# Kernel optimization log

Hardware: AMD Instinct MI355X
Metric: run time of the kernel (lower is better)

## Reference

```python
import jax, jax.numpy as jnp
import numpy as np

N, NFEAT, HID, NHEADS, NCLASS = 6144, 128, 128, 8, 40
SMOOTH = 0.5   # smoo init arg of GC_withres
ALPHA = 0.2    # LeakyReLU negative slope (pyGAT default)
EPS = 1e-5     # BatchNorm eps
NEG = -9e15    # masked-attention fill value


def setup_inputs() -> dict:
    key = jax.random.key(0)
    ks = jax.random.split(key, 20)
    x = jax.random.normal(ks[0], (N, NFEAT), dtype=jnp.float32)
    # sparse-ish symmetric normalized adjacency (~12 avg degree + self loops)
    m = (jax.random.uniform(ks[1], (N, N)) < 0.001).astype(jnp.float32)
    a = jnp.maximum(m, m.T) + jnp.eye(N, dtype=jnp.float32)
    dinv = 1.0 / jnp.sqrt(jnp.sum(a, axis=1))
    adj = a * dinv[:, None] * dinv[None, :]
    W_att = jax.random.normal(ks[2], (NHEADS, NFEAT, HID), dtype=jnp.float32) * 0.1
    a_src = jax.random.normal(ks[3], (NHEADS, HID), dtype=jnp.float32) * 0.1
    a_dst = jax.random.normal(ks[4], (NHEADS, HID), dtype=jnp.float32) * 0.1
    bn0_g = jnp.ones((NFEAT,), jnp.float32)
    bn0_b = jnp.zeros((NFEAT,), jnp.float32)
    bn0_m = jax.random.normal(ks[5], (NFEAT,), dtype=jnp.float32) * 0.1
    bn0_v = 1.0 + 0.1 * jax.random.uniform(ks[6], (NFEAT,), dtype=jnp.float32)
    bn1_g = jnp.ones((HID,), jnp.float32)
    bn1_b = jnp.zeros((HID,), jnp.float32)
    bn1_m = jax.random.normal(ks[7], (HID,), dtype=jnp.float32) * 0.1
    bn1_v = 1.0 + 0.1 * jax.random.uniform(ks[8], (HID,), dtype=jnp.float32)
    gc_w = jax.random.normal(ks[9], (HID * NHEADS, NCLASS), dtype=jnp.float32) * 0.05
    gc_b = jnp.zeros((NCLASS,), jnp.float32)
    return {"x": x, "adj": adj, "W_att": W_att, "a_src": a_src, "a_dst": a_dst,
            "bn0_g": bn0_g, "bn0_b": bn0_b, "bn0_m": bn0_m, "bn0_v": bn0_v,
            "bn1_g": bn1_g, "bn1_b": bn1_b, "bn1_m": bn1_m, "bn1_v": bn1_v,
            "gc_w": gc_w, "gc_b": gc_b}


def _bn(x, g, b, m, v):
    # BatchNorm1d in eval mode: normalize with running stats
    return (x - m) * (g / jnp.sqrt(v + EPS)) + b


def reference(x, adj, W_att, a_src, a_dst, bn0_g, bn0_b, bn0_m, bn0_v,
              bn1_g, bn1_b, bn1_m, bn1_v, gc_w, gc_b):
    x = _bn(x, bn0_g, bn0_b, bn0_m, bn0_v)          # bn0; dropout identity (eval)
    mask = adj > 0
    head_outs = []
    for h in range(NHEADS):                          # fixed small head count
        Wh = x @ W_att[h]                            # [N, HID]
        s1 = Wh @ a_src[h]                           # [N]
        s2 = Wh @ a_dst[h]                           # [N]
        e = jax.nn.leaky_relu(s1[:, None] + s2[None, :], ALPHA)  # [N, N]
        att = jax.nn.softmax(jnp.where(mask, e, NEG), axis=1)    # softmax over nbrs
        h_prime = att @ Wh                           # aggregate
        head_outs.append(jax.nn.relu(_bn(h_prime, bn1_g, bn1_b, bn1_m, bn1_v)))
    xcat = jnp.concatenate(head_outs, axis=1)        # [N, HID*NHEADS]
    # GC_withres: (smooth * A @ (XW) + XW) / (1 + smooth) + bias
    support = xcat @ gc_w                            # [N, NCLASS]
    out = (SMOOTH * (adj @ support) + support) / (1.0 + SMOOTH) + gc_b
    return jax.nn.log_softmax(out, axis=1)
```

## Files before the change

kernel.cpp:

```cpp
#include <hip/hip_runtime.h>
#include <math.h>

#define N      6144
#define NFEAT  128
#define HID    128
#define NHEADS 8
#define NCLASS 40
#define CAP    96
#define EPS    1e-5f
#define ALPHA  0.2f

typedef short bf16x8 __attribute__((ext_vector_type(8)));
typedef float f32x4  __attribute__((ext_vector_type(4)));

__device__ inline float bf2f(unsigned short u) {
  unsigned int x = ((unsigned int)u) << 16;
  return __builtin_bit_cast(float, x);
}
__device__ inline unsigned short f2bf(float f) {
  unsigned int x = __builtin_bit_cast(unsigned int, f);
  x += 0x7fffu + ((x >> 16) & 1u);
  return (unsigned short)(x >> 16);
}

__global__ __launch_bounds__(256) void prep_ell_kernel(
    const float* __restrict__ adj,
    int* __restrict__ cols, float* __restrict__ vals, int* __restrict__ cnt,
    const float* __restrict__ x,
    const float* __restrict__ g, const float* __restrict__ b,
    const float* __restrict__ m, const float* __restrict__ v,
    const float* __restrict__ Wall,
    unsigned short* __restrict__ xb, unsigned short* __restrict__ wbt) {
  __shared__ int scnt;
  if (blockIdx.x < N) {
    const int i = blockIdx.x;
    if (threadIdx.x == 0) scnt = 0;
    __syncthreads();
    const float* row = adj + (size_t)i * N;
    for (int j4 = threadIdx.x * 4; j4 < N; j4 += 1024) {
      float4 a = *(const float4*)(row + j4);
#pragma unroll
      for (int u = 0; u < 4; ++u) {
        float av = (u == 0) ? a.x : (u == 1) ? a.y : (u == 2) ? a.z : a.w;
        if (av > 0.f) {
          int s = atomicAdd(&scnt, 1);
          if (s < CAP) {
            cols[(size_t)i * CAP + s] = j4 + u;
            vals[(size_t)i * CAP + s] = av;
          }
        }
      }
    }
    __syncthreads();
    if (threadIdx.x == 0) cnt[i] = min(scnt, CAP);
  } else {
    int idx = (blockIdx.x - N) * 256 + threadIdx.x;
    if (idx < N * NFEAT) {
      int c = idx & (NFEAT - 1);
      float sc = g[c] * rsqrtf(v[c] + EPS);
      xb[idx] = f2bf((x[idx] - m[c]) * sc + b[c]);
    } else {
      int t = idx - N * NFEAT;
      int h = t >> 14, nk = t & 16383, n = nk >> 7, k = nk & 127;
      wbt[t] = f2bf(Wall[(h << 14) + (k << 7) + n]);
    }
  }
}

__global__ __launch_bounds__(256) void gemm_score(
    const unsigned short* __restrict__ xb,
    const unsigned short* __restrict__ wbt,
    const float* __restrict__ a_src, const float* __restrict__ a_dst,
    unsigned short* __restrict__ whc,
    float* __restrict__ s1, float* __restrict__ s2) {
  const int h  = blockIdx.y;
  const int rb = blockIdx.x * 64;
  __shared__ unsigned short As[64][136];
  __shared__ unsigned short Bs[128][136];
  __shared__ float s1p[64], s2p[64];
  const int tid = threadIdx.x;

  if (tid < 64) { s1p[tid] = 0.f; s2p[tid] = 0.f; }
#pragma unroll
  for (int r = 0; r < 4; ++r) {
    int chunk = tid + r * 256;
    int row = chunk >> 4, c8 = (chunk & 15) * 8;
    *(uint4*)&As[row][c8] = *(const uint4*)(xb + (size_t)(rb + row) * NFEAT + c8);
  }
  const unsigned short* W = wbt + h * (HID * NFEAT);
#pragma unroll
  for (int r = 0; r < 8; ++r) {
    int chunk = tid + r * 256;
    int row = chunk >> 4, c8 = (chunk & 15) * 8;
    *(uint4*)&Bs[row][c8] = *(const uint4*)(W + (size_t)row * NFEAT + c8);
  }
  __syncthreads();

  const int wid = tid >> 6, l = tid & 63, lm = l & 15, lq = l >> 4;
  const int cw = wid * 32;
  f32x4 acc[4][2] = {};
#pragma unroll
  for (int kk = 0; kk < NFEAT; kk += 32) {
    bf16x8 af[4], bfr[2];
#pragma unroll
    for (int mt = 0; mt < 4; ++mt)
      af[mt] = *(const bf16x8*)&As[mt * 16 + lm][kk + lq * 8];
#pragma unroll
    for (int nt = 0; nt < 2; ++nt)
      bfr[nt] = *(const bf16x8*)&Bs[cw + nt * 16 + lm][kk + lq * 8];
#pragma unroll
    for (int mt = 0; mt < 4; ++mt)
#pragma unroll
      for (int nt = 0; nt < 2; ++nt)
        acc[mt][nt] = __builtin_amdgcn_mfma_f32_16x16x32_bf16(
            af[mt], bfr[nt], acc[mt][nt], 0, 0, 0);
  }

  unsigned short* C = whc + (size_t)h * HID;
#pragma unroll
  for (int mt = 0; mt < 4; ++mt)
#pragma unroll
    for (int nt = 0; nt < 2; ++nt)
#pragma unroll
      for (int r = 0; r < 4; ++r)
        C[(size_t)(rb + mt * 16 + lq * 4 + r) * (NHEADS * HID)
          + cw + nt * 16 + lm] = f2bf(acc[mt][nt][r]);

  const float as0 = a_src[h * HID + cw + lm];
  const float as1 = a_src[h * HID + cw + 16 + lm];
  const float ad0 = a_dst[h * HID + cw + lm];
  const float ad1 = a_dst[h * HID + cw + 16 + lm];
#pragma unroll
  for (int mt = 0; mt < 4; ++mt)
#pragma unroll
    for (int r = 0; r < 4; ++r) {
      float p1 = acc[mt][0][r] * as0 + acc[mt][1][r] * as1;
      float p2 = acc[mt][0][r] * ad0 + acc[mt][1][r] * ad1;
#pragma unroll
      for (int off = 1; off < 16; off <<= 1) {
        p1 += __shfl_xor(p1, off, 64);
        p2 += __shfl_xor(p2, off, 64);
      }
      if (lm == 0) {
        atomicAdd(&s1p[mt * 16 + lq * 4 + r], p1);
        atomicAdd(&s2p[mt * 16 + lq * 4 + r], p2);
      }
    }
  __syncthreads();
  if (tid < 64) {
    s1[(size_t)h * N + rb + tid] = s1p[tid];
    s2[(size_t)h * N + rb + tid] = s2p[tid];
  }
}

__global__ __launch_bounds__(256) void attn_kernel(
    const unsigned short* __restrict__ whc,
    const float* __restrict__ s1, const float* __restrict__ s2,
    const int* __restrict__ cols, const int* __restrict__ cnt,
    const float* __restrict__ g, const float* __restrict__ b,
    const float* __restrict__ m, const float* __restrict__ v,
    float* __restrict__ xcat) {
  const int i = blockIdx.x, t = threadIdx.x;
  __shared__ int   jsh[CAP + 2];
  __shared__ float wsh[NHEADS][CAP + 2];
  __shared__ float ssum[NHEADS];
  __shared__ float accsh[128][9];

  const int c = cnt[i];
  const int cpad = (c + 1) & ~1;
  if (t < CAP + 2) jsh[t] = (t < c) ? cols[(size_t)i * CAP + t] : 0;
  if (t < 16) wsh[t >> 1][c + (t & 1)] = 0.f;
  __syncthreads();

  if (t < 128) {
    const int h = t >> 4, u = t & 15;
    const float si = s1[(size_t)h * N + i];
    const float* s2h = s2 + (size_t)h * N;
    float mx = -INFINITY;
    for (int e = u; e < c; e += 16) {
      float val = si + s2h[jsh[e]];
      val = val >= 0.f ? val : ALPHA * val;
      mx = fmaxf(mx, val);
    }
#pragma unroll
    for (int off = 1; off < 16; off <<= 1) mx = fmaxf(mx, __shfl_xor(mx, off, 64));
    float sm = 0.f;
    for (int e = u; e < c; e += 16) {
      float val = si + s2h[jsh[e]];
      val = val >= 0.f ? val : ALPHA * val;
      float wv = expf(val - mx);
      wsh[h][e] = wv;
      sm += wv;
    }
#pragma unroll
    for (int off = 1; off < 16; off <<= 1) sm += __shfl_xor(sm, off, 64);
    if (u == 0) ssum[h] = sm;
  }
  __syncthreads();

  const int p  = t >> 7;
  const int q  = t & 127;
  const int f0 = q * 8;
  const int hh = q >> 4;
  float acc[8] = {0.f, 0.f, 0.f, 0.f, 0.f, 0.f, 0.f, 0.f};
  for (int e = 0; e < cpad; e += 2) {
    const int   j = jsh[e + p];
    const float w = wsh[hh][e + p];
    uint4 U = *(const uint4*)(whc + (size_t)j * (NHEADS * HID) + f0);
    acc[0] += w * bf2f((unsigned short)(U.x & 0xffff));
    acc[1] += w * bf2f((unsigned short)(U.x >> 16));
    acc[2] += w * bf2f((unsigned short)(U.y & 0xffff));
    acc[3] += w * bf2f((unsigned short)(U.y >> 16));
    acc[4] += w * bf2f((unsigned short)(U.z & 0xffff));
    acc[5] += w * bf2f((unsigned short)(U.z >> 16));
    acc[6] += w * bf2f((unsigned short)(U.w & 0xffff));
    acc[7] += w * bf2f((unsigned short)(U.w >> 16));
  }
  if (p == 1) {
#pragma unroll
    for (int j = 0; j < 8; ++j) accsh[q][j] = acc[j];
  }
  __syncthreads();
  if (p == 0) {
    const float inv = 1.f / ssum[hh];
    const int ch0 = (q & 15) * 8;
    float4 gv0 = *(const float4*)(g + ch0), gv1 = *(const float4*)(g + ch0 + 4);
    float4 bv0 = *(const float4*)(b + ch0), bv1 = *(const float4*)(b + ch0 + 4);
    float4 mv0 = *(const float4*)(m + ch0), mv1 = *(const float4*)(m + ch0 + 4);
    float4 vv0 = *(const float4*)(v + ch0), vv1 = *(const float4*)(v + ch0 + 4);
    float gg[8] = {gv0.x, gv0.y, gv0.z, gv0.w, gv1.x, gv1.y, gv1.z, gv1.w};
    float bb[8] = {bv0.x, bv0.y, bv0.z, bv0.w, bv1.x, bv1.y, bv1.z, bv1.w};
    float mm[8] = {mv0.x, mv0.y, mv0.z, mv0.w, mv1.x, mv1.y, mv1.z, mv1.w};
    float vv[8] = {vv0.x, vv0.y, vv0.z, vv0.w, vv1.x, vv1.y, vv1.z, vv1.w};
    float o[8];
#pragma unroll
    for (int j = 0; j < 8; ++j) {
      float hp = (acc[j] + accsh[q][j]) * inv;
      o[j] = fmaxf((hp - mm[j]) * (gg[j] * rsqrtf(vv[j] + EPS)) + bb[j], 0.f);
    }
    float* xr = xcat + (size_t)i * (NHEADS * HID) + f0;
    float4 o0 = {o[0], o[1], o[2], o[3]}, o1 = {o[4], o[5], o[6], o[7]};
    *(float4*)xr = o0;
    *(float4*)(xr + 4) = o1;
  }
}

__global__ __launch_bounds__(256) void support_kernel(
    const float* __restrict__ xcat, const float* __restrict__ gcw,
    float* __restrict__ sup) {
  int wave = (blockIdx.x * 256 + threadIdx.x) >> 6;
  int lane = threadIdx.x & 63;
  int cc = lane < NCLASS ? lane : NCLASS - 1;
  const float* x0 = xcat + (size_t)(wave * 2 + 0) * (NHEADS * HID);
  const float* x1 = xcat + (size_t)(wave * 2 + 1) * (NHEADS * HID);
  float a0 = 0.f, a1 = 0.f;
#pragma unroll 4
  for (int k = 0; k < NHEADS * HID; k += 4) {
    float4 v0 = *(const float4*)(x0 + k);
    float4 v1 = *(const float4*)(x1 + k);
    float w0 = gcw[(size_t)(k + 0) * NCLASS + cc];
    float w1 = gcw[(size_t)(k + 1) * NCLASS + cc];
    float w2 = gcw[(size_t)(k + 2) * NCLASS + cc];
    float w3 = gcw[(size_t)(k + 3) * NCLASS + cc];
    a0 += v0.x * w0 + v0.y * w1 + v0.z * w2 + v0.w * w3;
    a1 += v1.x * w0 + v1.y * w1 + v1.z * w2 + v1.w * w3;
  }
  if (lane < NCLASS) {
    sup[(size_t)(wave * 2 + 0) * NCLASS + lane] = a0;
    sup[(size_t)(wave * 2 + 1) * NCLASS + lane] = a1;
  }
}

__global__ __launch_bounds__(64) void final_kernel(
    const float* __restrict__ sup,
    const int* __restrict__ cols, const float* __restrict__ vals,
    const int* __restrict__ cnt, const float* __restrict__ gcb,
    float* __restrict__ out) {
  const int i = blockIdx.x, t = threadIdx.x;
  const bool act = t < NCLASS;
  const int c = cnt[i];
  const int* cl = cols + (size_t)i * CAP;
  const float* vl = vals + (size_t)i * CAP;
  float s = act ? sup[(size_t)i * NCLASS + t] : 0.f;
  float agg = 0.f;
  for (int e = 0; e < c; ++e) {
    int j = cl[e];
    float a = vl[e];
    if (act) agg += a * sup[(size_t)j * NCLASS + t];
  }
  float o = act ? ((0.5f * agg + s) * (1.f / 1.5f) + gcb[t]) : -INFINITY;
  float mx = o;
#pragma unroll
  for (int off = 32; off; off >>= 1) mx = fmaxf(mx, __shfl_xor(mx, off, 64));
  float ex = act ? expf(o - mx) : 0.f;
#pragma unroll
  for (int off = 32; off; off >>= 1) ex += __shfl_xor(ex, off, 64);
  if (act) out[(size_t)i * NCLASS + t] = o - mx - logf(ex);
}

extern "C" void kernel_launch(void* const* d_in, const int* in_sizes, int n_in,
                              void* d_out, int out_size, void* d_ws, size_t ws_size,
                              hipStream_t stream) {
  const float* x     = (const float*)d_in[0];
  const float* adj   = (const float*)d_in[1];
  const float* W_att = (const float*)d_in[2];
  const float* a_src = (const float*)d_in[3];
  const float* a_dst = (const float*)d_in[4];
  const float* bn0_g = (const float*)d_in[5];
  const float* bn0_b = (const float*)d_in[6];
  const float* bn0_m = (const float*)d_in[7];
  const float* bn0_v = (const float*)d_in[8];
  const float* bn1_g = (const float*)d_in[9];
  const float* bn1_b = (const float*)d_in[10];
  const float* bn1_m = (const float*)d_in[11];
  const float* bn1_v = (const float*)d_in[12];
  const float* gc_w  = (const float*)d_in[13];
  const float* gc_b  = (const float*)d_in[14];
  float* out = (float*)d_out;
  (void)in_sizes; (void)n_in; (void)out_size; (void)ws_size;

  char* w = (char*)d_ws;
  unsigned short* xb  = (unsigned short*)w; w += (size_t)N * NFEAT * 2;
  unsigned short* wbt = (unsigned short*)w; w += (size_t)NHEADS * NFEAT * HID * 2;
  unsigned short* whc = (unsigned short*)w; w += (size_t)N * NHEADS * HID * 2;
  float* s1   = (float*)w; w += (size_t)NHEADS * N * 4;
  float* s2   = (float*)w; w += (size_t)NHEADS * N * 4;
  float* xcat = (float*)w; w += (size_t)N * NHEADS * HID * 4;
  float* sup  = (float*)w; w += (size_t)N * NCLASS * 4;
  float* vals = (float*)w; w += (size_t)N * CAP * 4;
  int*   cols = (int*)w;   w += (size_t)N * CAP * 4;
  int*   cnt  = (int*)w;   w += (size_t)N * 4;

  const int prep_blocks = (N * NFEAT + NHEADS * NFEAT * HID) / 256;
  prep_ell_kernel<<<dim3(N + prep_blocks), dim3(256), 0, stream>>>(
      adj, cols, vals, cnt, x, bn0_g, bn0_b, bn0_m, bn0_v, W_att, xb, wbt);
  gemm_score<<<dim3(N / 64, NHEADS), dim3(256), 0, stream>>>(
      xb, wbt, a_src, a_dst, whc, s1, s2);
  attn_kernel<<<dim3(N), dim3(256), 0, stream>>>(
      whc, s1, s2, cols, cnt, bn1_g, bn1_b, bn1_m, bn1_v, xcat);
  support_kernel<<<dim3((N / 2) * 64 / 256), dim3(256), 0, stream>>>(
      xcat, gc_w, sup);
  final_kernel<<<dim3(N), dim3(64), 0, stream>>>(
      sup, cols, vals, cnt, gc_b, out);
}
```

Before: 361.0 us.

## Store xcat as bf16 and compute support GEMM with MFMA

The attention kernel now writes its concatenated head outputs as bf16 instead of fp32, halving that intermediate's memory traffic. The scalar FMA support GEMM is replaced by an MFMA 16x16x32 bf16 kernel. It reads a transposed bf16 copy of gc_w, padded to 48 classes and built in the prep kernel. This targets the support matmul's compute and bandwidth cost, at the price of bf16 rounding on xcat and gc_w.

```diff
diff --git a/kernel.cpp b/kernel.cpp
--- a/kernel.cpp
+++ b/kernel.cpp
@@ -6,6 +6,7 @@
 #define HID    128
 #define NHEADS 8
 #define NCLASS 40
+#define NCPAD  48
 #define CAP    96
 #define EPS    1e-5f
 #define ALPHA  0.2f
@@ -29,8 +30,9 @@
     const float* __restrict__ x,
     const float* __restrict__ g, const float* __restrict__ b,
     const float* __restrict__ m, const float* __restrict__ v,
-    const float* __restrict__ Wall,
-    unsigned short* __restrict__ xb, unsigned short* __restrict__ wbt) {
+    const float* __restrict__ Wall, const float* __restrict__ gcw,
+    unsigned short* __restrict__ xb, unsigned short* __restrict__ wbt,
+    unsigned short* __restrict__ gctb) {
   __shared__ int scnt;
   if (blockIdx.x < N) {
     const int i = blockIdx.x;
@@ -59,10 +61,14 @@
       int c = idx & (NFEAT - 1);
       float sc = g[c] * rsqrtf(v[c] + EPS);
       xb[idx] = f2bf((x[idx] - m[c]) * sc + b[c]);
-    } else {
+    } else if (idx < N * NFEAT + NHEADS * NFEAT * HID) {
       int t = idx - N * NFEAT;
       int h = t >> 14, nk = t & 16383, n = nk >> 7, k = nk & 127;
       wbt[t] = f2bf(Wall[(h << 14) + (k << 7) + n]);
+    } else {
+      int t = idx - N * NFEAT - NHEADS * NFEAT * HID;
+      int cls = t >> 10, k = t & 1023;
+      gctb[t] = (cls < NCLASS) ? f2bf(gcw[k * NCLASS + cls]) : (unsigned short)0;
     }
   }
 }
@@ -159,7 +165,7 @@
     const int* __restrict__ cols, const int* __restrict__ cnt,
     const float* __restrict__ g, const float* __restrict__ b,
     const float* __restrict__ m, const float* __restrict__ v,
-    float* __restrict__ xcat) {
+    unsigned short* __restrict__ xcatb) {
   const int i = blockIdx.x, t = threadIdx.x;
   __shared__ int   jsh[CAP + 2];
   __shared__ float wsh[NHEADS][CAP + 2];
@@ -232,43 +238,45 @@
     float bb[8] = {bv0.x, bv0.y, bv0.z, bv0.w, bv1.x, bv1.y, bv1.z, bv1.w};
     float mm[8] = {mv0.x, mv0.y, mv0.z, mv0.w, mv1.x, mv1.y, mv1.z, mv1.w};
     float vv[8] = {vv0.x, vv0.y, vv0.z, vv0.w, vv1.x, vv1.y, vv1.z, vv1.w};
-    float o[8];
+    unsigned short ob[8];
 #pragma unroll
     for (int j = 0; j < 8; ++j) {
       float hp = (acc[j] + accsh[q][j]) * inv;
-      o[j] = fmaxf((hp - mm[j]) * (gg[j] * rsqrtf(vv[j] + EPS)) + bb[j], 0.f);
-    }
-    float* xr = xcat + (size_t)i * (NHEADS * HID) + f0;
-    float4 o0 = {o[0], o[1], o[2], o[3]}, o1 = {o[4], o[5], o[6], o[7]};
-    *(float4*)xr = o0;
-    *(float4*)(xr + 4) = o1;
-  }
-}
-
-__global__ __launch_bounds__(256) void support_kernel(
-    const float* __restrict__ xcat, const float* __restrict__ gcw,
+      ob[j] = f2bf(fmaxf((hp - mm[j]) * (gg[j] * rsqrtf(vv[j] + EPS)) + bb[j], 0.f));
+    }
+    uint4 U;
+    U.x = (unsigned int)ob[0] | ((unsigned int)ob[1] << 16);
+    U.y = (unsigned int)ob[2] | ((unsigned int)ob[3] << 16);
+    U.z = (unsigned int)ob[4] | ((unsigned int)ob[5] << 16);
+    U.w = (unsigned int)ob[6] | ((unsigned int)ob[7] << 16);
+    *(uint4*)(xcatb + (size_t)i * (NHEADS * HID) + f0) = U;
+  }
+}
+
+__global__ __launch_bounds__(256) void support_mfma(
+    const unsigned short* __restrict__ xcatb,
+    const unsigned short* __restrict__ gctb,
     float* __restrict__ sup) {
-  int wave = (blockIdx.x * 256 + threadIdx.x) >> 6;
-  int lane = threadIdx.x & 63;
-  int cc = lane < NCLASS ? lane : NCLASS - 1;
-  const float* x0 = xcat + (size_t)(wave * 2 + 0) * (NHEADS * HID);
-  const float* x1 = xcat + (size_t)(wave * 2 + 1) * (NHEADS * HID);
-  float a0 = 0.f, a1 = 0.f;
-#pragma unroll 4
-  for (int k = 0; k < NHEADS * HID; k += 4) {
-    float4 v0 = *(const float4*)(x0 + k);
-    float4 v1 = *(const float4*)(x1 + k);
-    float w0 = gcw[(size_t)(k + 0) * NCLASS + cc];
-    float w1 = gcw[(size_t)(k + 1) * NCLASS + cc];
-    float w2 = gcw[(size_t)(k + 2) * NCLASS + cc];
-    float w3 = gcw[(size_t)(k + 3) * NCLASS + cc];
-    a0 += v0.x * w0 + v0.y * w1 + v0.z * w2 + v0.w * w3;
-    a1 += v1.x * w0 + v1.y * w1 + v1.z * w2 + v1.w * w3;
-  }
-  if (lane < NCLASS) {
-    sup[(size_t)(wave * 2 + 0) * NCLASS + lane] = a0;
-    sup[(size_t)(wave * 2 + 1) * NCLASS + lane] = a1;
-  }
+  const int wv = (blockIdx.x * 256 + threadIdx.x) >> 6;
+  const int l = threadIdx.x & 63, lm = l & 15, lq = l >> 4;
+  const int rb = wv * 16;
+  f32x4 acc[3] = {};
+  for (int kk = 0; kk < NHEADS * HID; kk += 32) {
+    bf16x8 a = *(const bf16x8*)(xcatb + (size_t)(rb + lm) * (NHEADS * HID) + kk + lq * 8);
+#pragma unroll
+    for (int nt = 0; nt < 3; ++nt) {
+      bf16x8 bb = *(const bf16x8*)(gctb + (size_t)(nt * 16 + lm) * (NHEADS * HID) + kk + lq * 8);
+      acc[nt] = __builtin_amdgcn_mfma_f32_16x16x32_bf16(a, bb, acc[nt], 0, 0, 0);
+    }
+  }
+#pragma unroll
+  for (int nt = 0; nt < 3; ++nt)
+#pragma unroll
+    for (int r = 0; r < 4; ++r) {
+      int col = nt * 16 + lm;
+      if (col < NCLASS)
+        sup[(size_t)(rb + lq * 4 + r) * NCLASS + col] = acc[nt][r];
+    }
 }
 
 __global__ __launch_bounds__(64) void final_kernel(
@@ -320,26 +328,29 @@
   (void)in_sizes; (void)n_in; (void)out_size; (void)ws_size;
 
   char* w = (char*)d_ws;
-  unsigned short* xb  = (unsigned short*)w; w += (size_t)N * NFEAT * 2;
-  unsigned short* wbt = (unsigned short*)w; w += (size_t)NHEADS * NFEAT * HID * 2;
-  unsigned short* whc = (unsigned short*)w; w += (size_t)N * NHEADS * HID * 2;
+  unsigned short* xb    = (unsigned short*)w; w += (size_t)N * NFEAT * 2;
+  unsigned short* wbt   = (unsigned short*)w; w += (size_t)NHEADS * NFEAT * HID * 2;
+  unsigned short* whc   = (unsigned short*)w; w += (size_t)N * NHEADS * HID * 2;
+  unsigned short* xcatb = (unsigned short*)w; w += (size_t)N * NHEADS * HID * 2;
+  unsigned short* gctb  = (unsigned short*)w; w += (size_t)NCPAD * NHEADS * HID * 2;
   float* s1   = (float*)w; w += (size_t)NHEADS * N * 4;
   float* s2   = (float*)w; w += (size_t)NHEADS * N * 4;
-  float* xcat = (float*)w; w += (size_t)N * NHEADS * HID * 4;
   float* sup  = (float*)w; w += (size_t)N * NCLASS * 4;
   float* vals = (float*)w; w += (size_t)N * CAP * 4;
   int*   cols = (int*)w;   w += (size_t)N * CAP * 4;
   int*   cnt  = (int*)w;   w += (size_t)N * 4;
 
-  const int prep_blocks = (N * NFEAT + NHEADS * NFEAT * HID) / 256;
+  const int prep_blocks =
+      (N * NFEAT + NHEADS * NFEAT * HID + NCPAD * NHEADS * HID) / 256;
   prep_ell_kernel<<<dim3(N + prep_blocks), dim3(256), 0, stream>>>(
-      adj, cols, vals, cnt, x, bn0_g, bn0_b, bn0_m, bn0_v, W_att, xb, wbt);
+      adj, cols, vals, cnt, x, bn0_g, bn0_b, bn0_m, bn0_v, W_att, gc_w,
+      xb, wbt, gctb);
   gemm_score<<<dim3(N / 64, NHEADS), dim3(256), 0, stream>>>(
       xb, wbt, a_src, a_dst, whc, s1, s2);
   attn_kernel<<<dim3(N), dim3(256), 0, stream>>>(
-      whc, s1, s2, cols, cnt, bn1_g, bn1_b, bn1_m, bn1_v, xcat);
-  support_kernel<<<dim3((N / 2) * 64 / 256), dim3(256), 0, stream>>>(
-      xcat, gc_w, sup);
+      whc, s1, s2, cols, cnt, bn1_g, bn1_b, bn1_m, bn1_v, xcatb);
+  support_mfma<<<dim3(N / 16 / 4), dim3(256), 0, stream>>>(
+      xcatb, gctb, sup);
   final_kernel<<<dim3(N), dim3(64), 0, stream>>>(
       sup, cols, vals, cnt, gc_b, out);
 }
```

New measurement: 303.5 us, median of 2. -15.9%, faster.
